# Kernel tuning notes

Hardware: AMD Instinct MI355X
Metric: run time of the kernel (lower is better)

Reference implementation:

```python
import jax, jax.numpy as jnp
import numpy as np

K = 51           # kernel_size
DENSE_INNER = 2
EPS_LN = 1e-6
EPS_GRN = 1e-6

def _make_peripheral_coords(radius, dense_inner=2):
    coords = list(range(0, min(radius, dense_inner) + 1))
    v = 1
    while v < radius:
        v *= 2
        if v > dense_inner and v < radius:
            coords.append(v)
    if radius not in coords:
        coords.append(radius)
    return sorted(set(coords))

def _quantise(a, coords):
    q = 0
    for c in coords:
        if c <= a:
            q = c
        else:
            break
    return q

def _build_idx_map(kernel_size, dense_inner):
    radius = kernel_size // 2
    coords = _make_peripheral_coords(radius, dense_inner)
    signed = [-c for c in reversed(coords[1:])] + list(coords)
    P = len(signed)
    c2i = {c: i for i, c in enumerate(signed)}
    idx = []
    for i in range(kernel_size):
        oi = i - radius
        qi = _quantise(abs(oi), coords)
        ii = c2i[-qi if oi < 0 else qi]
        for j in range(kernel_size):
            oj = j - radius
            qj = _quantise(abs(oj), coords)
            jj = c2i[-qj if oj < 0 else qj]
            idx.append(ii * P + jj)
    return np.asarray(idx, dtype=np.int32), P

IDX_MAP, P = _build_idx_map(K, DENSE_INNER)  # P == 13 for K=51

DIM = 384
HID = 4 * DIM

def setup_inputs() -> dict:
    key = jax.random.key(0)
    ks = jax.random.split(key, 10)
    B, C, H, W = 8, DIM, 64, 64
    std = 0.02
    return {
        "x": jax.random.normal(ks[0], (B, C, H, W), jnp.float32),
        "weight_comp": jax.random.normal(ks[1], (C, P * P), jnp.float32) * std,
        "kpe": jax.random.normal(ks[2], (1, 1, K, K), jnp.float32) * std,
        "ln_w": jnp.ones((C,), jnp.float32),
        "ln_b": jnp.zeros((C,), jnp.float32),
        "w1": jax.random.normal(ks[3], (C, HID), jnp.float32) * std,
        "b1": jnp.zeros((HID,), jnp.float32),
        "grn_gamma": jax.random.normal(ks[4], (HID,), jnp.float32) * std,
        "grn_beta": jax.random.normal(ks[5], (HID,), jnp.float32) * std,
        "w2": jax.random.normal(ks[6], (HID, C), jnp.float32) * std,
        "b2": jnp.zeros((C,), jnp.float32),
    }

def _block(x, weight_comp, kpe, ln_w, ln_b, w1, b1, grn_gamma, grn_beta, w2, b2):
    C = x.shape[1]
    # gather-built peripheral depthwise kernel: (C, 1, K, K) + shared positional bias
    w = weight_comp[:, IDX_MAP].reshape(C, 1, K, K) + kpe
    y = jax.lax.conv_general_dilated(
        x, w, window_strides=(1, 1), padding=[(K // 2, K // 2)] * 2,
        feature_group_count=C, dimension_numbers=("NCHW", "OIHW", "NCHW"))
    h = y.transpose(0, 2, 3, 1)  # NHWC
    # LayerNorm (channels_last, biased variance, eps=1e-6)
    mu = jnp.mean(h, axis=-1, keepdims=True)
    var = jnp.mean(jnp.square(h - mu), axis=-1, keepdims=True)
    h = (h - mu) * jax.lax.rsqrt(var + EPS_LN) * ln_w + ln_b
    # pointwise MLP with GRN
    h = jnp.einsum("nhwc,cf->nhwf", h, w1) + b1
    h = jax.nn.gelu(h, approximate=False)  # nn.GELU default is exact erf form
    gx = jnp.sqrt(jnp.sum(jnp.square(h), axis=(1, 2), keepdims=True))  # (N,1,1,F)
    nx = gx / (jnp.mean(gx, axis=-1, keepdims=True) + EPS_GRN)
    h = grn_gamma * (h * nx) + grn_beta + h
    h = jnp.einsum("nhwf,fc->nhwc", h, w2) + b2
    return x + h.transpose(0, 3, 1, 2)

def reference(x, weight_comp, kpe, ln_w, ln_b, w1, b1, grn_gamma, grn_beta, w2, b2):
    return _block(x, weight_comp, kpe, ln_w, ln_b, w1, b1, grn_gamma, grn_beta, w2, b2)
```

## Files before the change

### kernel.cpp

```cpp
#include <hip/hip_runtime.h>

#define CDIM 384
#define FDIM 1536
#define KK 51
#define RAD 25
#define NPIX 32768
#define HW 4096

#define CSTR 136
#define OSTR 68

typedef float  f32x4  __attribute__((ext_vector_type(4)));
typedef short  short8 __attribute__((ext_vector_type(8)));
typedef __bf16 bf16x8 __attribute__((ext_vector_type(8)));
typedef unsigned short us4 __attribute__((ext_vector_type(4)));

__device__ __constant__ int AXIS[51] = {
  0,
  1,1,1,1,1,1,1,1,1,
  2,2,2,2,2,2,2,2,
  3,3,3,3,
  4,4,
  5,
  6,
  7,
  8,8,
  9,9,9,9,
  10,10,10,10,10,10,10,10,
  11,11,11,11,11,11,11,11,11,
  12
};

__device__ __forceinline__ unsigned short bf16_rn(float x){
  union { float f; unsigned u; } v; v.f = x;
  unsigned r = v.u + 0x7FFFu + ((v.u >> 16) & 1u);
  return (unsigned short)(r >> 16);
}
__device__ __forceinline__ unsigned short f2bf(float x){
  __bf16 h = (__bf16)x;
  return __builtin_bit_cast(unsigned short, h);
}
__device__ __forceinline__ float bf2f(unsigned short h){
  union { unsigned u; float f; } v; v.u = ((unsigned)h) << 16; return v.f;
}
__device__ __forceinline__ float gelu_f(float v){
  float t = v*(0.7978845608f + 0.0356774081f*v*v);
  float sg = 1.f/(1.f + __expf(-2.f*t));
  return v * sg;
}

__global__ __launch_bounds__(256) void k_prep(const float* __restrict__ wc,
                                              const float* __restrict__ kpe,
                                              float* __restrict__ wfull,
                                              const float* __restrict__ w1,
                                              unsigned short* __restrict__ w1T,
                                              const float* __restrict__ w2,
                                              unsigned short* __restrict__ w2T,
                                              const float* __restrict__ beta,
                                              const float* __restrict__ b2,
                                              float* __restrict__ c2,
                                              float* __restrict__ grn){
  __shared__ float tile[64][65];
  __shared__ float red[256];
  int bid = blockIdx.x;
  int tid = threadIdx.x;
  if (bid < 384){
    int c = bid;
    const float* wcc = wc + c*169;
    float* wo = wfull + (size_t)c*2601;
    for (int idx = tid; idx < 2601; idx += 256){
      int i = idx / 51, j = idx - i*51;
      wo[idx] = wcc[AXIS[i]*13 + AXIS[j]] + kpe[idx];
    }
  } else if (bid < 672){
    const float* src; unsigned short* dst; int R, C, t;
    if (bid < 528){ src = w1; dst = w1T; R = CDIM; C = FDIM; t = bid - 384; }
    else          { src = w2; dst = w2T; R = FDIM; C = CDIM; t = bid - 528; }
    int nct = C >> 6;
    int tc = t % nct, tr = t / nct;
    int r0 = tr*64, c0 = tc*64;
    int lane = tid & 63, q = tid >> 6;
    #pragma unroll
    for (int it = 0; it < 16; ++it){
      int r = it*4 + q;
      tile[r][lane] = src[(size_t)(r0 + r)*C + c0 + lane];
    }
    __syncthreads();
    #pragma unroll
    for (int it = 0; it < 16; ++it){
      int c = it*4 + q;
      dst[(size_t)(c0 + c)*R + r0 + lane] = f2bf(tile[lane][c]);
    }
  } else if (bid < 678){
    int lane = tid & 63, w = tid >> 6;
    int c = (bid - 672)*64 + lane;
    float s = 0.f;
    for (int f = w*384; f < (w + 1)*384; ++f)
      s += beta[f] * w2[(size_t)f*CDIM + c];
    red[w*64 + lane] = s;
    __syncthreads();
    if (tid < 64){
      float t = red[tid] + red[64 + tid] + red[128 + tid] + red[192 + tid];
      c2[c] = t + b2[c];
    }
  } else {
    for (int i = tid; i < 8*FDIM; i += 256) grn[i] = 0.f;
  }
}

__global__ __launch_bounds__(256) void k_conv_mfma(const float* __restrict__ x,
                                                   const float* __restrict__ wfull,
                                                   float* __restrict__ y){
  __shared__ __align__(16) float outb[64*OSTR];
  __shared__ __align__(16) unsigned short bufs[2][4][1088];
  int img = blockIdx.x;
  int ch  = img % CDIM;
  const float* xim = x + (size_t)img*HW;
  const float* wch = wfull + (size_t)ch*2601;
  int tid = threadIdx.x;
  int lane = tid & 63, wid = tid >> 6;
  int li = lane & 15, g = lane >> 4;
  int t0 = (lane & 31) << 2;
  int c0 = lane >> 5;

  for (int i = tid; i < 1088; i += 256)
    *(f32x4*)&outb[i*4] = (f32x4){0.f,0.f,0.f,0.f};

  bf16x8 Bf[4][2];
  #pragma unroll
  for (int nt = 0; nt < 4; ++nt){
    int i = nt*16 + li;
    #pragma unroll
    for (int kt = 0; kt < 2; ++kt){
      union { bf16x8 v; unsigned short u[8]; } tmp;
      #pragma unroll
      for (int e = 0; e < 8; ++e){
        int j = kt*32 + g*8 + e;
        float v = (i < 51 && j < 51) ? wch[i*51 + j] : 0.f;
        tmp.u[e] = bf16_rn(v);
      }
      Bf[nt][kt] = tmp.v;
    }
  }

  {
    const float* xr = xim + (16*wid)*64;
    #pragma unroll
    for (int it = 0; it < 4; ++it){
      int c = c0 + 2*it;
      us4 o;
      #pragma unroll
      for (int e = 0; e < 4; ++e){
        int xi = t0 + e + c - 25;
        float v = (xi >= 0 && xi < 64) ? xr[xi] : 0.f;
        o[e] = bf16_rn(v);
      }
      *(us4*)&bufs[0][wid][c*CSTR + t0] = o;
    }
  }
  __syncthreads();

  #pragma unroll 1
  for (int ph = 0; ph < 16; ++ph){
    float pf[16];
    if (ph + 1 < 16){
      const float* xr = xim + (ph + 1 + 16*wid)*64;
      #pragma unroll
      for (int it = 0; it < 4; ++it){
        int c = c0 + 2*it;
        #pragma unroll
        for (int e = 0; e < 4; ++e){
          int xi = t0 + e + c - 25;
          int xc = min(max(xi, 0), 63);
          pf[it*4 + e] = xr[xc];
        }
      }
    }

    bf16x8 Af[4][2];
    #pragma unroll
    for (int s = 0; s < 4; ++s){
      const unsigned short* bb = &bufs[ph & 1][s][0];
      #pragma unroll
      for (int kt = 0; kt < 2; ++kt){
        int u0 = wid*16 + kt*32 + g*8 + li;
        int c  = li & 7;
        Af[s][kt] = *(const bf16x8*)&bb[c*CSTR + (u0 - c)];
      }
    }

    #pragma unroll
    for (int dd = 0; dd < 6; ++dd){
      int d = dd - 2;
      int pmax = ph + 25 + 16*d;
      if (pmax < 0 || pmax > 78) continue;
      f32x4 V = {0.f,0.f,0.f,0.f};
      #pragma unroll
      for (int s = 0; s < 4; ++s){
        int nt = s - d;
        if (nt < 0 || nt > 3) continue;
        V = __builtin_amdgcn_mfma_f32_16x16x32_bf16(Af[s][0], Bf[nt][0], V, 0, 0, 0);
        V = __builtin_amdgcn_mfma_f32_16x16x32_bf16(Af[s][1], Bf[nt][1], V, 0, 0, 0);
      }
      int p = pmax - li;
      if (p >= 0 && p < 64){
        float* oa = &outb[p*OSTR + wid*16 + g*4];
        f32x4 old = *(const f32x4*)oa;
        *(f32x4*)oa = old + V;
      }
    }

    if (ph + 1 < 16){
      unsigned short* dst = &bufs[(ph + 1) & 1][wid][0];
      #pragma unroll
      for (int it = 0; it < 4; ++it){
        int c = c0 + 2*it;
        us4 o;
        #pragma unroll
        for (int e = 0; e < 4; ++e){
          int xi = t0 + e + c - 25;
          float v = (xi >= 0 && xi < 64) ? pf[it*4 + e] : 0.f;
          o[e] = bf16_rn(v);
        }
        *(us4*)&dst[c*CSTR + t0] = o;
      }
    }
    __syncthreads();
  }

  float* yo = y + (size_t)img*HW;
  #pragma unroll
  for (int k = 0; k < 4; ++k){
    int pix = k*1024 + tid*4;
    int p = pix >> 6, q = pix & 63;
    *(f32x4*)(yo + pix) = *(const f32x4*)&outb[p*OSTR + q];
  }
}

__global__ __launch_bounds__(256) void k_gemm1p(const float* __restrict__ y,
                                                const float* __restrict__ lnw,
                                                const float* __restrict__ lnb,
                                                const unsigned short* __restrict__ BT,
                                                const float* __restrict__ b1,
                                                unsigned short* __restrict__ H,
                                                float* __restrict__ grn){
  __shared__ __align__(16) unsigned short pan[64*392];
  __shared__ __align__(16) unsigned short bS[2][128*40];
  __shared__ float sred[2][4][64];
  int m0 = blockIdx.x * 64;
  int img = m0 >> 12;
  int tid = threadIdx.x;
  int lane = tid & 63, wid = tid >> 6;
  int wr = wid >> 1, wc = wid & 1;
  int lm = lane & 15, g = lane >> 4;
  int sr = tid & 127, sc = tid >> 7;

  {
    int sp0 = m0 & 4095;
    const float* yb = y + (size_t)img*CDIM*HW + sp0 + lane;
    int cbase = wid*96;
    float v[96];
    float sum = 0.f, sq = 0.f;
    #pragma unroll
    for (int cc = 0; cc < 96; ++cc){
      float t = yb[(size_t)(cbase + cc)*HW];
      v[cc] = t; sum += t; sq += t*t;
    }
    sred[0][wid][lane] = sum; sred[1][wid][lane] = sq;
    __syncthreads();
    float ts = 0.f, tq = 0.f;
    #pragma unroll
    for (int u = 0; u < 4; ++u){ ts += sred[0][u][lane]; tq += sred[1][u][lane]; }
    float mu   = ts * (1.f/CDIM);
    float rstd = rsqrtf(tq * (1.f/CDIM) - mu*mu + 1e-6f);
    #pragma unroll
    for (int j = 0; j < 12; ++j){
      short8 o;
      #pragma unroll
      for (int e = 0; e < 8; ++e){
        int c = cbase + j*8 + e;
        float t = (v[j*8 + e] - mu) * rstd * lnw[c] + lnb[c];
        o[e] = (short)f2bf(t);
      }
      *(short8*)&pan[lane*392 + cbase + j*8] = o;
    }
  }

  {
    const unsigned short* gb = BT + (size_t)sr*CDIM + sc*16;
    *(short8*)&bS[0][sr*40 + sc*16]     = *(const short8*)(gb);
    *(short8*)&bS[0][sr*40 + sc*16 + 8] = *(const short8*)(gb + 8);
  }
  short8 rn0, rn1;
  {
    const unsigned short* gb = BT + (size_t)sr*CDIM + 32 + sc*16;
    rn0 = *(const short8*)(gb);
    rn1 = *(const short8*)(gb + 8);
  }
  int pft = 0, pk = 64;
  int par = 0;

  #pragma unroll 1
  for (int ft = 0; ft < 12; ++ft){
    f32x4 acc[2][4];
    #pragma unroll
    for (int i = 0; i < 2; ++i)
      #pragma unroll
      for (int j = 0; j < 4; ++j) acc[i][j] = (f32x4){0.f,0.f,0.f,0.f};

    #pragma unroll 1
    for (int ks = 0; ks < 12; ++ks){
      int k0 = ks*32;
      __syncthreads();
      if (!(ft == 11 && ks == 11)){
        *(short8*)&bS[par^1][sr*40 + sc*16]     = rn0;
        *(short8*)&bS[par^1][sr*40 + sc*16 + 8] = rn1;
      }
      if (!(ft == 11 && ks >= 10)){
        const unsigned short* gb = BT + (size_t)(pft*128 + sr)*CDIM + pk + sc*16;
        rn0 = *(const short8*)(gb);
        rn1 = *(const short8*)(gb + 8);
        pk += 32; if (pk == CDIM){ pk = 0; ++pft; }
      }
      bf16x8 aF[2], bF[4];
      #pragma unroll
      for (int fm = 0; fm < 2; ++fm) aF[fm] = *(const bf16x8*)&pan[(wr*32 + fm*16 + lm)*392 + k0 + g*8];
      #pragma unroll
      for (int fn = 0; fn < 4; ++fn) bF[fn] = *(const bf16x8*)&bS[par][(wc*64 + fn*16 + lm)*40 + g*8];
      #pragma unroll
      for (int fm = 0; fm < 2; ++fm)
        #pragma unroll
        for (int fn = 0; fn < 4; ++fn)
          acc[fm][fn] = __builtin_amdgcn_mfma_f32_16x16x32_bf16(aF[fm], bF[fn], acc[fm][fn], 0, 0, 0);
      par ^= 1;
    }

    int n0 = ft*128;
    float psum[4] = {0.f,0.f,0.f,0.f};
    #pragma unroll
    for (int fn = 0; fn < 4; ++fn){
      int n = n0 + wc*64 + fn*16 + lm;
      float bias = b1[n];
      #pragma unroll
      for (int fm = 0; fm < 2; ++fm){
        int mb = m0 + wr*32 + fm*16 + g*4;
        #pragma unroll
        for (int r = 0; r < 4; ++r){
          float v = gelu_f(acc[fm][fn][r] + bias);
          H[(size_t)(mb + r)*FDIM + n] = f2bf(v);
          psum[fn] += v*v;
        }
      }
    }
    #pragma unroll
    for (int fn = 0; fn < 4; ++fn){
      float v = psum[fn];
      v += __shfl_xor(v, 16);
      v += __shfl_xor(v, 32);
      if (g == 0){
        atomicAdd(&grn[img*FDIM + n0 + wc*64 + fn*16 + lm], v);
      }
    }
  }
}

__global__ __launch_bounds__(256) void k_grn(const float* __restrict__ grn,
                                             const float* __restrict__ gamma,
                                             float* __restrict__ S){
  int n = blockIdx.x;
  const float* g = grn + n*FDIM;
  __shared__ float red[256];
  float p = 0.f;
  for (int f = threadIdx.x; f < FDIM; f += 256) p += sqrtf(g[f]);
  red[threadIdx.x] = p;
  __syncthreads();
  for (int s = 128; s > 0; s >>= 1){
    if (threadIdx.x < s) red[threadIdx.x] += red[threadIdx.x + s];
    __syncthreads();
  }
  float mean = red[0] * (1.f/FDIM);
  float inv = 1.f/(mean + 1e-6f);
  for (int f = threadIdx.x; f < FDIM; f += 256){
    float nx = sqrtf(g[f]) * inv;
    S[n*FDIM + f] = 1.f + gamma[f]*nx;
  }
}

__global__ __launch_bounds__(256) void k_scale(const unsigned short* __restrict__ w2T,
                                               const float* __restrict__ S,
                                               unsigned short* __restrict__ W2s){
  int img = blockIdx.y;
  size_t base = ((size_t)blockIdx.x*256 + threadIdx.x)*8;
  int f0 = (int)(base % FDIM);
  const float* Si = S + img*FDIM + f0;
  short8 wv = *(const short8*)(w2T + base);
  short8 o;
  #pragma unroll
  for (int e = 0; e < 8; ++e)
    o[e] = (short)f2bf(bf2f((unsigned short)wv[e]) * Si[e]);
  *(short8*)(W2s + (size_t)img*CDIM*FDIM + base) = o;
}

__global__ __launch_bounds__(256) void k_gemm2(const unsigned short* __restrict__ W2s,
                                               const unsigned short* __restrict__ H,
                                               const float* __restrict__ c2,
                                               const float* __restrict__ xg,
                                               float* __restrict__ out){
  __shared__ __align__(16) unsigned short aS[2][128*40];
  __shared__ __align__(16) unsigned short bS[2][128*40];
  int bid = blockIdx.x;
  int x8 = bid & 7;
  int kk = bid >> 3;
  int bm = kk % 3;
  int bn = x8 + 8*(kk / 3);
  int c0 = bm*128, p0 = bn*128;
  int img = p0 >> 12;
  const unsigned short* Wimg = W2s + (size_t)img*CDIM*FDIM;
  int tid = threadIdx.x;
  int lane = tid & 63, wid = tid >> 6;
  int wr = wid >> 1, wc = wid & 1;
  int lm = lane & 15, g = lane >> 4;
  int sr = tid & 127, sc = tid >> 7;
  f32x4 acc[4][4];
  #pragma unroll
  for (int i = 0; i < 4; ++i)
    #pragma unroll
    for (int j = 0; j < 4; ++j) acc[i][j] = (f32x4){0.f,0.f,0.f,0.f};

  {
    const unsigned short* ga = Wimg + (size_t)(c0 + sr)*FDIM + sc*16;
    *(short8*)&aS[0][sr*40 + sc*16]     = *(const short8*)(ga);
    *(short8*)&aS[0][sr*40 + sc*16 + 8] = *(const short8*)(ga + 8);
    const unsigned short* gb = H + (size_t)(p0 + sr)*FDIM + sc*16;
    *(short8*)&bS[0][sr*40 + sc*16]     = *(const short8*)(gb);
    *(short8*)&bS[0][sr*40 + sc*16 + 8] = *(const short8*)(gb + 8);
  }
  short8 ra0, ra1, rh0, rh1;
  {
    const unsigned short* ga = Wimg + (size_t)(c0 + sr)*FDIM + 32 + sc*16;
    ra0 = *(const short8*)(ga); ra1 = *(const short8*)(ga + 8);
    const unsigned short* gb = H + (size_t)(p0 + sr)*FDIM + 32 + sc*16;
    rh0 = *(const short8*)(gb); rh1 = *(const short8*)(gb + 8);
  }
  int par = 0;

  #pragma unroll 1
  for (int ks = 0; ks < 48; ++ks){
    __syncthreads();
    if (ks + 1 < 48){
      *(short8*)&aS[par^1][sr*40 + sc*16]     = ra0;
      *(short8*)&aS[par^1][sr*40 + sc*16 + 8] = ra1;
      *(short8*)&bS[par^1][sr*40 + sc*16]     = rh0;
      *(short8*)&bS[par^1][sr*40 + sc*16 + 8] = rh1;
    }
    if (ks + 2 < 48){
      int nk = (ks + 2)*32;
      const unsigned short* ga = Wimg + (size_t)(c0 + sr)*FDIM + nk + sc*16;
      ra0 = *(const short8*)(ga); ra1 = *(const short8*)(ga + 8);
      const unsigned short* gb = H + (size_t)(p0 + sr)*FDIM + nk + sc*16;
      rh0 = *(const short8*)(gb); rh1 = *(const short8*)(gb + 8);
    }
    bf16x8 aF[4], bF[4];
    #pragma unroll
    for (int fm = 0; fm < 4; ++fm) aF[fm] = *(const bf16x8*)&aS[par][(wr*64 + fm*16 + lm)*40 + g*8];
    #pragma unroll
    for (int fn = 0; fn < 4; ++fn) bF[fn] = *(const bf16x8*)&bS[par][(wc*64 + fn*16 + lm)*40 + g*8];
    #pragma unroll
    for (int fm = 0; fm < 4; ++fm)
      #pragma unroll
      for (int fn = 0; fn < 4; ++fn)
        acc[fm][fn] = __builtin_amdgcn_mfma_f32_16x16x32_bf16(aF[fm], bF[fn], acc[fm][fn], 0, 0, 0);
    par ^= 1;
  }

  int sp0 = p0 & 4095;
  #pragma unroll
  for (int fn = 0; fn < 4; ++fn){
    int pixoff = sp0 + wc*64 + fn*16 + lm;
    #pragma unroll
    for (int fm = 0; fm < 4; ++fm){
      #pragma unroll
      for (int r = 0; r < 4; ++r){
        int c = c0 + wr*64 + fm*16 + g*4 + r;
        size_t addr = ((size_t)img*CDIM + c)*HW + pixoff;
        out[addr] = acc[fm][fn][r] + c2[c] + xg[addr];
      }
    }
  }
}

extern "C" void kernel_launch(void* const* d_in, const int* in_sizes, int n_in,
                              void* d_out, int out_size, void* d_ws, size_t ws_size,
                              hipStream_t stream) {
  const float* x    = (const float*)d_in[0];
  const float* wc   = (const float*)d_in[1];
  const float* kpe  = (const float*)d_in[2];
  const float* lnw  = (const float*)d_in[3];
  const float* lnb  = (const float*)d_in[4];
  const float* w1   = (const float*)d_in[5];
  const float* b1   = (const float*)d_in[6];
  const float* gam  = (const float*)d_in[7];
  const float* beta = (const float*)d_in[8];
  const float* w2   = (const float*)d_in[9];
  const float* b2   = (const float*)d_in[10];
  float* out = (float*)d_out;

  char* ws = (char*)d_ws;
  size_t o = 0;
  auto take = [&](size_t bytes)->char*{
    char* p = ws + o;
    o = (o + bytes + 511) & ~(size_t)511;
    return p;
  };
  float*          y     = out;
  float*          wfull = (float*)take((size_t)CDIM*2601*4);
  unsigned short* H     = (unsigned short*)take((size_t)NPIX*FDIM*2);
  unsigned short* w1T   = (unsigned short*)take((size_t)CDIM*FDIM*2);
  unsigned short* w2T   = (unsigned short*)take((size_t)CDIM*FDIM*2);
  unsigned short* W2s   = (unsigned short*)take((size_t)8*CDIM*FDIM*2);
  float*          grn   = (float*)take(8*FDIM*4);
  float*          S     = (float*)take(8*FDIM*4);
  float*          c2    = (float*)take(CDIM*4);
  if (o > ws_size) return;

  k_prep<<<679, 256, 0, stream>>>(wc, kpe, wfull, w1, w1T, w2, w2T, beta, b2, c2, grn);
  k_conv_mfma<<<3072, 256, 0, stream>>>(x, wfull, y);
  k_gemm1p<<<NPIX/64, 256, 0, stream>>>(y, lnw, lnb, w1T, b1, H, grn);
  k_grn<<<8, 256, 0, stream>>>(grn, gam, S);
  k_scale<<<dim3(288, 8), 256, 0, stream>>>(w2T, S, W2s);
  k_gemm2<<<3*(NPIX/128), 256, 0, stream>>>(W2s, H, c2, x, out);
}
```

Measured before the change: 373.2 us.

## Halve gemm1 row tile and single-buffer conv input staging

New measurement: 471.1 us. +26.2%, slower.

```diff
diff --git a/kernel.cpp b/kernel.cpp
--- a/kernel.cpp
+++ b/kernel.cpp
@@ -112,7 +112,7 @@
                                                    const float* __restrict__ wfull,
                                                    float* __restrict__ y){
   __shared__ __align__(16) float outb[64*OSTR];
-  __shared__ __align__(16) unsigned short bufs[2][4][1088];
+  __shared__ __align__(16) unsigned short buf[4][1088];
   int img = blockIdx.x;
   int ch  = img % CDIM;
   const float* xim = x + (size_t)img*HW;
@@ -155,7 +155,7 @@
         float v = (xi >= 0 && xi < 64) ? xr[xi] : 0.f;
         o[e] = bf16_rn(v);
       }
-      *(us4*)&bufs[0][wid][c*CSTR + t0] = o;
+      *(us4*)&buf[wid][c*CSTR + t0] = o;
     }
   }
   __syncthreads();
@@ -180,7 +180,7 @@
     bf16x8 Af[4][2];
     #pragma unroll
     for (int s = 0; s < 4; ++s){
-      const unsigned short* bb = &bufs[ph & 1][s][0];
+      const unsigned short* bb = &buf[s][0];
       #pragma unroll
       for (int kt = 0; kt < 2; ++kt){
         int u0 = wid*16 + kt*32 + g*8 + li;
@@ -210,8 +210,9 @@
       }
     }
 
+    __syncthreads();
     if (ph + 1 < 16){
-      unsigned short* dst = &bufs[(ph + 1) & 1][wid][0];
+      unsigned short* dst = &buf[wid][0];
       #pragma unroll
       for (int it = 0; it < 4; ++it){
         int c = c0 + 2*it;
@@ -244,10 +245,10 @@
                                                 const float* __restrict__ b1,
                                                 unsigned short* __restrict__ H,
                                                 float* __restrict__ grn){
-  __shared__ __align__(16) unsigned short pan[64*392];
+  __shared__ __align__(16) unsigned short pan[32*392];
   __shared__ __align__(16) unsigned short bS[2][128*40];
-  __shared__ float sred[2][4][64];
-  int m0 = blockIdx.x * 64;
+  __shared__ float sred[2][8][32];
+  int m0 = blockIdx.x * 32;
   int img = m0 >> 12;
   int tid = threadIdx.x;
   int lane = tid & 63, wid = tid >> 6;
@@ -257,24 +258,26 @@
 
   {
     int sp0 = m0 & 4095;
-    const float* yb = y + (size_t)img*CDIM*HW + sp0 + lane;
-    int cbase = wid*96;
-    float v[96];
+    int px = lane & 31;
+    int cg = wid*2 + (lane >> 5);
+    int cbase = cg*48;
+    const float* yb = y + (size_t)img*CDIM*HW + sp0 + px;
+    float v[48];
     float sum = 0.f, sq = 0.f;
     #pragma unroll
-    for (int cc = 0; cc < 96; ++cc){
+    for (int cc = 0; cc < 48; ++cc){
       float t = yb[(size_t)(cbase + cc)*HW];
       v[cc] = t; sum += t; sq += t*t;
     }
-    sred[0][wid][lane] = sum; sred[1][wid][lane] = sq;
+    sred[0][cg][px] = sum; sred[1][cg][px] = sq;
     __syncthreads();
     float ts = 0.f, tq = 0.f;
     #pragma unroll
-    for (int u = 0; u < 4; ++u){ ts += sred[0][u][lane]; tq += sred[1][u][lane]; }
+    for (int u = 0; u < 8; ++u){ ts += sred[0][u][px]; tq += sred[1][u][px]; }
     float mu   = ts * (1.f/CDIM);
     float rstd = rsqrtf(tq * (1.f/CDIM) - mu*mu + 1e-6f);
     #pragma unroll
-    for (int j = 0; j < 12; ++j){
+    for (int j = 0; j < 6; ++j){
       short8 o;
       #pragma unroll
       for (int e = 0; e < 8; ++e){
@@ -282,7 +285,7 @@
         float t = (v[j*8 + e] - mu) * rstd * lnw[c] + lnb[c];
         o[e] = (short)f2bf(t);
       }
-      *(short8*)&pan[lane*392 + cbase + j*8] = o;
+      *(short8*)&pan[px*392 + cbase + j*8] = o;
     }
   }
 
@@ -302,11 +305,9 @@
 
   #pragma unroll 1
   for (int ft = 0; ft < 12; ++ft){
-    f32x4 acc[2][4];
-    #pragma unroll
-    for (int i = 0; i < 2; ++i)
-      #pragma unroll
-      for (int j = 0; j < 4; ++j) acc[i][j] = (f32x4){0.f,0.f,0.f,0.f};
+    f32x4 acc[4];
+    #pragma unroll
+    for (int j = 0; j < 4; ++j) acc[j] = (f32x4){0.f,0.f,0.f,0.f};
 
     #pragma unroll 1
     for (int ks = 0; ks < 12; ++ks){
@@ -322,16 +323,13 @@
         rn1 = *(const short8*)(gb + 8);
         pk += 32; if (pk == CDIM){ pk = 0; ++pft; }
       }
-      bf16x8 aF[2], bF[4];
-      #pragma unroll
-      for (int fm = 0; fm < 2; ++fm) aF[fm] = *(const bf16x8*)&pan[(wr*32 + fm*16 + lm)*392 + k0 + g*8];
+      bf16x8 aF, bF[4];
+      aF = *(const bf16x8*)&pan[(wr*16 + lm)*392 + k0 + g*8];
       #pragma unroll
       for (int fn = 0; fn < 4; ++fn) bF[fn] = *(const bf16x8*)&bS[par][(wc*64 + fn*16 + lm)*40 + g*8];
       #pragma unroll
-      for (int fm = 0; fm < 2; ++fm)
-        #pragma unroll
-        for (int fn = 0; fn < 4; ++fn)
-          acc[fm][fn] = __builtin_amdgcn_mfma_f32_16x16x32_bf16(aF[fm], bF[fn], acc[fm][fn], 0, 0, 0);
+      for (int fn = 0; fn < 4; ++fn)
+        acc[fn] = __builtin_amdgcn_mfma_f32_16x16x32_bf16(aF, bF[fn], acc[fn], 0, 0, 0);
       par ^= 1;
     }
 
@@ -341,15 +339,12 @@
     for (int fn = 0; fn < 4; ++fn){
       int n = n0 + wc*64 + fn*16 + lm;
       float bias = b1[n];
-      #pragma unroll
-      for (int fm = 0; fm < 2; ++fm){
-        int mb = m0 + wr*32 + fm*16 + g*4;
-        #pragma unroll
-        for (int r = 0; r < 4; ++r){
-          float v = gelu_f(acc[fm][fn][r] + bias);
-          H[(size_t)(mb + r)*FDIM + n] = f2bf(v);
-          psum[fn] += v*v;
-        }
+      int mb = m0 + wr*16 + g*4;
+      #pragma unroll
+      for (int r = 0; r < 4; ++r){
+        float v = gelu_f(acc[fn][r] + bias);
+        H[(size_t)(mb + r)*FDIM + n] = f2bf(v);
+        psum[fn] += v*v;
       }
     }
     #pragma unroll
@@ -525,7 +520,7 @@
 
   k_prep<<<679, 256, 0, stream>>>(wc, kpe, wfull, w1, w1T, w2, w2T, beta, b2, c2, grn);
   k_conv_mfma<<<3072, 256, 0, stream>>>(x, wfull, y);
-  k_gemm1p<<<NPIX/64, 256, 0, stream>>>(y, lnw, lnb, w1T, b1, H, grn);
+  k_gemm1p<<<NPIX/32, 256, 0, stream>>>(y, lnw, lnb, w1T, b1, H, grn);
   k_grn<<<8, 256, 0, stream>>>(grn, gam, S);
   k_scale<<<dim3(288, 8), 256, 0, stream>>>(w2T, S, W2s);
   k_gemm2<<<3*(NPIX/128), 256, 0, stream>>>(W2s, H, c2, x, out);
```
